# Kernel tuning notes

Measured on AMD Instinct MI355X. Metric: run time of the kernel, lower is better.

The kernel has to match this reference:

```python
import jax, jax.numpy as jnp
import numpy as np
import math
from jax import lax

IN_CH = 512
OUT_CH = 512
STYLE_DIM = 512
K = 3
BATCH = 8
H = W = 64


def setup_inputs() -> dict:
    key = jax.random.key(0)
    k1, k2, k3, k4 = jax.random.split(key, 4)
    x = jax.random.normal(k1, (BATCH, IN_CH, H, W), dtype=jnp.float32)
    style = jax.random.normal(k2, (BATCH, STYLE_DIM), dtype=jnp.float32)
    # learned params
    weight = jax.random.normal(k3, (OUT_CH, IN_CH, K, K), dtype=jnp.float32)
    mod_w = jax.random.normal(k4, (IN_CH, STYLE_DIM), dtype=jnp.float32) * (1.0 / math.sqrt(STYLE_DIM))
    return {"x": x, "style": style, "weight": weight, "mod_w": mod_w}


def reference(x, style, weight, mod_w):
    batch, in_ch, h, w = x.shape
    out_ch, _, k, _ = weight.shape
    scale = 1.0 / math.sqrt(in_ch * k * k)
    # style modulation: Linear(style_dim -> in_channels), no bias
    s = style @ mod_w.T                          # [B, Cin]
    # per-sample modulated weight: [B, Cout, Cin, k, k]
    wmod = scale * weight[None] * s[:, None, :, None, None]
    # demodulation
    demod = lax.rsqrt(jnp.sum(wmod * wmod, axis=(2, 3, 4)) + 1e-8)  # [B, Cout]
    wmod = wmod * demod[:, :, None, None, None]
    pad = k // 2

    def conv_one(xb, wb):
        # xb: [Cin,H,W], wb: [Cout,Cin,k,k]
        return lax.conv_general_dilated(
            xb[None], wb, window_strides=(1, 1),
            padding=[(pad, pad), (pad, pad)],
            dimension_numbers=("NCHW", "OIHW", "NCHW"))[0]

    out = jax.vmap(conv_one)(x, wmod)            # [B, Cout, H, W]
    return out
```

## Files before the change

kernel.cpp:

```cpp
#include <hip/hip_runtime.h>
#include <hip/hip_bf16.h>


using Acc4  = __attribute__((ext_vector_type(4))) float;
using Frag8 = __attribute__((ext_vector_type(8))) short;

__device__ __forceinline__ void load_lds16(const void* g, void* l) {
  __builtin_amdgcn_global_load_lds((const __attribute__((address_space(1))) void*)g,
                                   (__attribute__((address_space(3))) void*)l, 16, 0, 0);
}

__global__ __launch_bounds__(256) void style_kernel(
    const float* __restrict__ style,
    const float* __restrict__ mod_w,
    float* __restrict__ s_out) {
  const int b    = blockIdx.y;
  const int wid  = threadIdx.x >> 6;
  const int lane = threadIdx.x & 63;
  const int c    = blockIdx.x * 4 + wid;
  const float4* mw = (const float4*)(mod_w + (size_t)c * 512);
  const float4* st = (const float4*)(style + (size_t)b * 512);
  float sum = 0.f;
#pragma unroll
  for (int i = 0; i < 2; ++i) {
    float4 m = mw[lane + i * 64];
    float4 s = st[lane + i * 64];
    sum += m.x * s.x + m.y * s.y + m.z * s.z + m.w * s.w;
  }
#pragma unroll
  for (int off = 32; off > 0; off >>= 1) sum += __shfl_xor(sum, off, 64);
  if (lane == 0) s_out[b * 512 + c] = sum;
}

__global__ __launch_bounds__(256) void modwrite_kernel(
    const float* __restrict__ weight,
    const float* __restrict__ s_in,
    __hip_bfloat16* __restrict__ wout) {
  const int o = blockIdx.x;
  const int b = blockIdx.y;
  __shared__ float ws[4608];
  __shared__ float s_lds[512];
  __shared__ float red[4];
  __shared__ float s_mult;
  const int tid  = threadIdx.x;
  const int lane = tid & 63;
  const int wid  = tid >> 6;

  for (int i = tid; i < 512; i += 256) s_lds[i] = s_in[b * 512 + i];
  __syncthreads();

  const float2* w2 = (const float2*)(weight + (size_t)o * 4608);
  float sum = 0.f;
#pragma unroll
  for (int i = 0; i < 9; ++i) {
    int idx = i * 256 + tid;
    float2 v = w2[idx];
    int e0 = idx * 2;
    int c0 = (e0 * 7282) >> 16;
    int c1 = ((e0 + 1) * 7282) >> 16;
    float a  = v.x * s_lds[c0];
    float bb = v.y * s_lds[c1];
    ws[e0] = a; ws[e0 + 1] = bb;
    sum += a * a + bb * bb;
  }
#pragma unroll
  for (int off = 32; off > 0; off >>= 1) sum += __shfl_xor(sum, off, 64);
  if (lane == 0) red[wid] = sum;
  __syncthreads();
  if (tid == 0) {
    const float scale = 1.4731391e-2f;
    float t = red[0] + red[1] + red[2] + red[3];
    s_mult = scale * rsqrtf(t * scale * scale + 1e-8f);
  }
  __syncthreads();
  const float mult = s_mult;
#pragma unroll
  for (int t = 0; t < 9; ++t) {
    __hip_bfloat16* orow = wout + (((size_t)b * 9 + t) * 512 + o) * 512;
#pragma unroll
    for (int i = 0; i < 2; ++i) {
      int c = i * 256 + tid;
      orow[c] = __float2bfloat16(ws[c * 9 + t] * mult);
    }
  }
}

__global__ __launch_bounds__(256) void transpose_kernel(
    const float* __restrict__ x,
    __hip_bfloat16* __restrict__ xbf) {
  __shared__ float t_lds[64][65];
  const int pt = blockIdx.x;
  const int ct = blockIdx.y;
  const int b  = blockIdx.z;
  const int tid  = threadIdx.x;
  const int lane = tid & 63;
  const int row4 = tid >> 6;
  const int c0 = ct * 64, p0 = pt * 64;
  const float* xb = x + ((size_t)b * 512 + c0) * 4096 + p0;
#pragma unroll
  for (int i = 0; i < 16; ++i) {
    int c = i * 4 + row4;
    t_lds[c][lane] = xb[(size_t)c * 4096 + lane];
  }
  __syncthreads();
  __hip_bfloat16* ob = xbf + ((size_t)b * 4096 + p0) * 512 + c0;
#pragma unroll
  for (int i = 0; i < 16; ++i) {
    int p = i * 4 + row4;
    ob[(size_t)p * 512 + lane] = __float2bfloat16(t_lds[lane][p]);
  }
}

#define X_OFF 0
#define W_OFF 32768

__global__ __launch_bounds__(256, 2) void conv_kernel(
    const __hip_bfloat16* __restrict__ xbf,
    const __hip_bfloat16* __restrict__ wmod,
    float* __restrict__ out) {
  __shared__ __align__(16) char lds[49152];
  const int ptile = blockIdx.x;
  const int otile = blockIdx.y;
  const int b     = blockIdx.z;
  const int tid  = threadIdx.x;
  const int lane = tid & 63;
  const int wid  = tid >> 6;
  const int wr   = wid >> 1, wc = wid & 1;
  const int y0   = ptile * 2;
  const int o0   = otile * 128;

  Acc4 acc[4][4] = {};
  const Frag8 zfrag = {0, 0, 0, 0, 0, 0, 0, 0};

  for (int cs = 0; cs < 8; ++cs) {
    const int c0 = cs * 64;
    __syncthreads();
#pragma unroll
    for (int i = 0; i < 8; ++i) {
      int chunk = i * 256 + tid;
      int pos = chunk >> 3;
      int ch  = chunk & 7;
      int gy  = y0 - 1 + (pos >> 6);
      gy = min(63, max(0, gy));
      int gx  = pos & 63;
      int sch = ch ^ (pos & 7);
      const __hip_bfloat16* src =
          xbf + (((size_t)b * 4096 + gy * 64 + gx) * 512 + c0 + sch * 8);
      load_lds16(src, lds + X_OFF + i * 4096 + wid * 1024);
    }
#pragma unroll
    for (int tap = 0; tap < 9; ++tap) {
      const int ky = tap / 3;
      const int kx = tap % 3;
      __syncthreads();
#pragma unroll
      for (int i = 0; i < 4; ++i) {
        int chunk = i * 256 + tid;
        int o   = chunk >> 3;
        int ch  = chunk & 7;
        int sch = ch ^ (o & 7);
        const __hip_bfloat16* src =
            wmod + ((((size_t)b * 9 + tap) * 512 + o0 + o) * 512 + c0 + sch * 8);
        load_lds16(src, lds + W_OFF + i * 4096 + wid * 1024);
      }
      __syncthreads();

      int  psv[4];
      bool valid[4];
#pragma unroll
      for (int n = 0; n < 4; ++n) {
        int plocal = wc * 64 + n * 16 + (lane & 15);
        int yrel = plocal >> 6;
        int xx   = plocal & 63;
        int sx   = xx + kx - 1;
        int sy   = y0 + yrel + ky - 1;
        valid[n] = ((unsigned)sx < 64u) && ((unsigned)sy < 64u);
        psv[n]   = (((yrel + ky) * 64 + sx) & 255);
      }
#pragma unroll
      for (int ks = 0; ks < 2; ++ks) {
        Frag8 af[4], bfr[4];
        const int chq = ks * 4 + (lane >> 4);
#pragma unroll
        for (int m = 0; m < 4; ++m) {
          int o = wr * 64 + m * 16 + (lane & 15);
          af[m] = *(const Frag8*)(lds + W_OFF + o * 128 + ((chq ^ (o & 7)) << 4));
        }
#pragma unroll
        for (int n = 0; n < 4; ++n) {
          int ps = psv[n];
          Frag8 v = *(const Frag8*)(lds + X_OFF + ps * 128 + ((chq ^ (ps & 7)) << 4));
          bfr[n] = valid[n] ? v : zfrag;
        }
#pragma unroll
        for (int m = 0; m < 4; ++m)
#pragma unroll
          for (int n = 0; n < 4; ++n)
            acc[m][n] = __builtin_amdgcn_mfma_f32_16x16x32_bf16(af[m], bfr[n], acc[m][n], 0, 0, 0);
      }
    }
  }

#pragma unroll
  for (int m = 0; m < 4; ++m) {
    int o = o0 + wr * 64 + m * 16 + ((lane >> 4) << 2);
#pragma unroll
    for (int n = 0; n < 4; ++n) {
      int p = ptile * 128 + wc * 64 + n * 16 + (lane & 15);
      float* dst = out + ((size_t)b * 512 + o) * 4096 + p;
#pragma unroll
      for (int j = 0; j < 4; ++j) dst[(size_t)j * 4096] = acc[m][n][j];
    }
  }
}

extern "C" void kernel_launch(void* const* d_in, const int* in_sizes, int n_in,
                              void* d_out, int out_size, void* d_ws, size_t ws_size,
                              hipStream_t stream) {
  const float* x      = (const float*)d_in[0];
  const float* style  = (const float*)d_in[1];
  const float* weight = (const float*)d_in[2];
  const float* mod_w  = (const float*)d_in[3];
  float* out = (float*)d_out;

  __hip_bfloat16* xbf  = (__hip_bfloat16*)d_ws;
  __hip_bfloat16* wmod = (__hip_bfloat16*)((char*)d_ws + (size_t)8 * 4096 * 512 * 2);
  float* s_buf = (float*)d_ws;

  style_kernel   <<<dim3(128, 8), 256, 0, stream>>>(style, mod_w, s_buf);
  modwrite_kernel<<<dim3(512, 8), 256, 0, stream>>>(weight, s_buf, wmod);
  transpose_kernel<<<dim3(64, 8, 8), 256, 0, stream>>>(x, xbf);
  conv_kernel    <<<dim3(32, 4, 8), 256, 0, stream>>>(xbf, wmod, out);
}
```

Baseline: 283.0 us.

## Double-buffer weight tiles in conv kernel, remap block order, vectorize prep stores

The conv kernel now double-buffers the per-tap weight tile in LDS, prefetching the next tap's weights while the current tap's MFMAs run. This replaces the two barriers per tap with one wait-and-barrier. The grid is flattened and block IDs are permuted so neighbouring blocks land on different XCD/L2 groups. The transpose and modwrite kernels now use float4 loads and packed bf16 stores. LDS grows to 64KB, which may lower occupancy at 2 blocks per CU.

```diff
diff --git a/kernel.cpp b/kernel.cpp
--- a/kernel.cpp
+++ b/kernel.cpp
@@ -74,14 +74,14 @@
   }
   __syncthreads();
   const float mult = s_mult;
+  const int c = tid * 2;
 #pragma unroll
   for (int t = 0; t < 9; ++t) {
     __hip_bfloat16* orow = wout + (((size_t)b * 9 + t) * 512 + o) * 512;
-#pragma unroll
-    for (int i = 0; i < 2; ++i) {
-      int c = i * 256 + tid;
-      orow[c] = __float2bfloat16(ws[c * 9 + t] * mult);
-    }
+    __hip_bfloat16 h0 = __float2bfloat16(ws[c * 9 + t] * mult);
+    __hip_bfloat16 h1 = __float2bfloat16(ws[(c + 1) * 9 + t] * mult);
+    ushort2 pk = { *(unsigned short*)&h0, *(unsigned short*)&h1 };
+    *(ushort2*)(orow + c) = pk;
   }
 }
 
@@ -92,22 +92,30 @@
   const int pt = blockIdx.x;
   const int ct = blockIdx.y;
   const int b  = blockIdx.z;
-  const int tid  = threadIdx.x;
-  const int lane = tid & 63;
-  const int row4 = tid >> 6;
+  const int tid = threadIdx.x;
+  const int l16 = tid & 15, g16 = tid >> 4;
   const int c0 = ct * 64, p0 = pt * 64;
   const float* xb = x + ((size_t)b * 512 + c0) * 4096 + p0;
 #pragma unroll
-  for (int i = 0; i < 16; ++i) {
-    int c = i * 4 + row4;
-    t_lds[c][lane] = xb[(size_t)c * 4096 + lane];
+  for (int i = 0; i < 4; ++i) {
+    int c = i * 16 + g16;
+    float4 v = *(const float4*)(xb + (size_t)c * 4096 + l16 * 4);
+    t_lds[c][l16 * 4 + 0] = v.x; t_lds[c][l16 * 4 + 1] = v.y;
+    t_lds[c][l16 * 4 + 2] = v.z; t_lds[c][l16 * 4 + 3] = v.w;
   }
   __syncthreads();
   __hip_bfloat16* ob = xbf + ((size_t)b * 4096 + p0) * 512 + c0;
 #pragma unroll
-  for (int i = 0; i < 16; ++i) {
-    int p = i * 4 + row4;
-    ob[(size_t)p * 512 + lane] = __float2bfloat16(t_lds[lane][p]);
+  for (int i = 0; i < 4; ++i) {
+    int p = i * 16 + g16;
+    int c = l16 * 4;
+    __hip_bfloat16 h0 = __float2bfloat16(t_lds[c + 0][p]);
+    __hip_bfloat16 h1 = __float2bfloat16(t_lds[c + 1][p]);
+    __hip_bfloat16 h2 = __float2bfloat16(t_lds[c + 2][p]);
+    __hip_bfloat16 h3 = __float2bfloat16(t_lds[c + 3][p]);
+    ushort4 pk = { *(unsigned short*)&h0, *(unsigned short*)&h1,
+                   *(unsigned short*)&h2, *(unsigned short*)&h3 };
+    *(ushort4*)(ob + (size_t)p * 512 + c) = pk;
   }
 }
 
@@ -118,10 +126,12 @@
     const __hip_bfloat16* __restrict__ xbf,
     const __hip_bfloat16* __restrict__ wmod,
     float* __restrict__ out) {
-  __shared__ __align__(16) char lds[49152];
-  const int ptile = blockIdx.x;
-  const int otile = blockIdx.y;
-  const int b     = blockIdx.z;
+  __shared__ __align__(16) char lds[65536];
+  const int bid  = blockIdx.x;
+  const int nid  = (bid & 7) * 128 + (bid >> 3);
+  const int ptile = nid & 31;
+  const int otile = (nid >> 5) & 3;
+  const int b     = nid >> 7;
   const int tid  = threadIdx.x;
   const int lane = tid & 63;
   const int wid  = tid >> 6;
@@ -132,39 +142,45 @@
   Acc4 acc[4][4] = {};
   const Frag8 zfrag = {0, 0, 0, 0, 0, 0, 0, 0};
 
-  for (int cs = 0; cs < 8; ++cs) {
+  auto stageX = [&](int cs) {
     const int c0 = cs * 64;
-    __syncthreads();
 #pragma unroll
     for (int i = 0; i < 8; ++i) {
       int chunk = i * 256 + tid;
-      int pos = chunk >> 3;
-      int ch  = chunk & 7;
-      int gy  = y0 - 1 + (pos >> 6);
-      gy = min(63, max(0, gy));
+      int pos = chunk >> 3, ch = chunk & 7;
+      int gy  = min(63, max(0, y0 - 1 + (pos >> 6)));
       int gx  = pos & 63;
       int sch = ch ^ (pos & 7);
-      const __hip_bfloat16* src =
-          xbf + (((size_t)b * 4096 + gy * 64 + gx) * 512 + c0 + sch * 8);
-      load_lds16(src, lds + X_OFF + i * 4096 + wid * 1024);
-    }
+      load_lds16(xbf + (((size_t)b * 4096 + gy * 64 + gx) * 512 + c0 + sch * 8),
+                 lds + X_OFF + i * 4096 + wid * 1024);
+    }
+  };
+  auto stageW = [&](int cs, int tap, int dst) {
+    const int c0 = cs * 64;
+#pragma unroll
+    for (int i = 0; i < 4; ++i) {
+      int chunk = i * 256 + tid;
+      int o = chunk >> 3, ch = chunk & 7;
+      int sch = ch ^ (o & 7);
+      load_lds16(wmod + ((((size_t)b * 9 + tap) * 512 + o0 + o) * 512 + c0 + sch * 8),
+                 lds + dst + i * 4096 + wid * 1024);
+    }
+  };
+
+  int woff = W_OFF;
+  stageX(0);
+  stageW(0, 0, woff);
+  asm volatile("s_waitcnt vmcnt(0)" ::: "memory");
+  __builtin_amdgcn_s_barrier();
+
+  for (int cs = 0; cs < 8; ++cs) {
 #pragma unroll
     for (int tap = 0; tap < 9; ++tap) {
+      if (tap < 8)           stageW(cs, tap + 1, woff ^ 16384);
+      else if (cs < 7)       stageW(cs + 1, 0, woff ^ 16384);
+
       const int ky = tap / 3;
       const int kx = tap % 3;
-      __syncthreads();
-#pragma unroll
-      for (int i = 0; i < 4; ++i) {
-        int chunk = i * 256 + tid;
-        int o   = chunk >> 3;
-        int ch  = chunk & 7;
-        int sch = ch ^ (o & 7);
-        const __hip_bfloat16* src =
-            wmod + ((((size_t)b * 9 + tap) * 512 + o0 + o) * 512 + c0 + sch * 8);
-        load_lds16(src, lds + W_OFF + i * 4096 + wid * 1024);
-      }
-      __syncthreads();
-
       int  psv[4];
       bool valid[4];
 #pragma unroll
@@ -184,7 +200,7 @@
 #pragma unroll
         for (int m = 0; m < 4; ++m) {
           int o = wr * 64 + m * 16 + (lane & 15);
-          af[m] = *(const Frag8*)(lds + W_OFF + o * 128 + ((chq ^ (o & 7)) << 4));
+          af[m] = *(const Frag8*)(lds + woff + o * 128 + ((chq ^ (o & 7)) << 4));
         }
 #pragma unroll
         for (int n = 0; n < 4; ++n) {
@@ -198,6 +214,17 @@
           for (int n = 0; n < 4; ++n)
             acc[m][n] = __builtin_amdgcn_mfma_f32_16x16x32_bf16(af[m], bfr[n], acc[m][n], 0, 0, 0);
       }
+
+      if (tap < 8) {
+        asm volatile("s_waitcnt vmcnt(0)" ::: "memory");
+        __builtin_amdgcn_s_barrier();
+      } else {
+        __builtin_amdgcn_s_barrier();
+        if (cs < 7) stageX(cs + 1);
+        asm volatile("s_waitcnt vmcnt(0)" ::: "memory");
+        __builtin_amdgcn_s_barrier();
+      }
+      woff ^= 16384;
     }
   }
 
@@ -227,8 +254,8 @@
   __hip_bfloat16* wmod = (__hip_bfloat16*)((char*)d_ws + (size_t)8 * 4096 * 512 * 2);
   float* s_buf = (float*)d_ws;
 
-  style_kernel   <<<dim3(128, 8), 256, 0, stream>>>(style, mod_w, s_buf);
-  modwrite_kernel<<<dim3(512, 8), 256, 0, stream>>>(weight, s_buf, wmod);
+  style_kernel    <<<dim3(128, 8), 256, 0, stream>>>(style, mod_w, s_buf);
+  modwrite_kernel <<<dim3(512, 8), 256, 0, stream>>>(weight, s_buf, wmod);
   transpose_kernel<<<dim3(64, 8, 8), 256, 0, stream>>>(x, xbf);
-  conv_kernel    <<<dim3(32, 4, 8), 256, 0, stream>>>(xbf, wmod, out);
-}
+  conv_kernel     <<<dim3(1024), 256, 0, stream>>>(xbf, wmod, out);
+}
```

After: 256.7 us. -9.3%, faster.
